# Kernel tuning notes

Hardware: AMD Instinct MI355X
Metric: run time of the kernel (lower is better)

The kernel has to match this reference:

```python
import jax, jax.numpy as jnp
import numpy as np

DIM = 256
WIN = 4
HEADS = 4
HEAD_DIM = DIM // HEADS
SCALE = HEAD_DIM ** (-0.5)


def setup_inputs() -> dict:
    key = jax.random.key(0)
    k1, k2, k3 = jax.random.split(key, 3)
    x = jax.random.normal(k1, (4, DIM, 32, 32, 32), dtype=jnp.float32)
    # xavier_uniform with gain=0.02 ~ small weights; scale approximated
    w_qkv = jax.random.normal(k2, (3 * DIM, DIM), dtype=jnp.float32) * 0.02
    w_proj = jax.random.normal(k3, (DIM, DIM), dtype=jnp.float32) * 0.02
    return {"x": x, "w_qkv": w_qkv, "w_proj": w_proj}


def reference(x, w_qkv, w_proj):
    B, C, D, H, W = x.shape
    N = D * H * W
    s = round(N ** (1.0 / 3.0))  # perfect cube asserted by original module
    w = WIN
    # (B,C,D,H,W) -> (B,N,C) -> (B,s,s,s,C)
    xt = x.reshape(B, C, N).transpose(0, 2, 1).reshape(B, s, s, s, C)
    pad = (w - s % w) % w
    if pad:
        xt = jnp.pad(xt, ((0, 0), (0, pad), (0, pad), (0, pad), (0, 0)))
    Sp = s + pad
    n = Sp // w  # windows per axis
    # torch unfold layout: (B, nD, nH, nW, C, w, w, w)
    xw = xt.reshape(B, n, w, n, w, n, w, C).transpose(0, 1, 3, 5, 7, 2, 4, 6)
    # faithful to torch .view(-1, w*w*w, C): row-major reinterpret of (C,w,w,w)
    xw = xw.reshape(-1, w * w * w, C)  # (nw, 64, C)
    nw, ntok = xw.shape[0], xw.shape[1]
    qkv = (xw @ w_qkv.T).reshape(nw, ntok, 3, HEADS, HEAD_DIM)
    q, k, v = qkv[:, :, 0], qkv[:, :, 1], qkv[:, :, 2]  # (nw, ntok, heads, hd)
    # faithful: NO head permute in original -> attention over the heads axis
    attn = jnp.einsum('wnhd,wngd->wnhg', q, k) * SCALE  # (nw, ntok, heads, heads)
    attn = jnp.clip(attn, -10.0, 10.0)
    attn = jax.nn.softmax(attn, axis=-1)
    out = jnp.einsum('wnhg,wngd->wnhd', attn, v)  # (nw, ntok, heads, hd)
    # faithful torch transpose(1,2).reshape(nw, ntok, dim)
    out = out.transpose(0, 2, 1, 3).reshape(nw, ntok, C)
    out = out @ w_proj.T
    out = out.reshape(B, n, n, n, w, w, w, C)
    out = out.transpose(0, 1, 4, 2, 5, 3, 6, 7).reshape(B, Sp, Sp, Sp, C)
    out = out[:, :s, :s, :s, :].transpose(0, 4, 1, 2, 3)  # (B,C,s,s,s)
    return out
```

## Files before the change

kernel.cpp:

```cpp
#include <hip/hip_runtime.h>

typedef _Float16 f16;
typedef f16 f16x2 __attribute__((ext_vector_type(2)));
typedef f16 f16x4 __attribute__((ext_vector_type(4)));
typedef f16 f16x8 __attribute__((ext_vector_type(8)));
typedef float f32x4 __attribute__((ext_vector_type(4)));

union v8split { f16x8 v8; f16x2 v2[4]; };

#define WQH_OFF 0
#define WPH_OFF (768 * 256 * 2)
#define XW_OFF  (WPH_OFF + 256 * 256 * 2)
#define O2_OFF  (XW_OFF + (size_t)2048 * 16384 * 2)
#define WS_NEED (O2_OFF + (size_t)2048 * 16384 * 2)

#define QKV_LDS_OFF 32768
#define SMEM_TOTAL 131072

__global__ __launch_bounds__(256) void cvt_weights_k(
    const float* __restrict__ wq, const float* __restrict__ wp,
    f16* __restrict__ wq_h, f16* __restrict__ wp_h) {
  int idx = blockIdx.x * 256 + threadIdx.x;
  if (idx < 768 * 256) wq_h[idx] = (f16)wq[idx];
  else wp_h[idx - 768 * 256] = (f16)wp[idx - 768 * 256];
}

__device__ __forceinline__ char* xwp(char* s, int row, int colbyte) {
  return s + row * 512 + (colbyte ^ (((row ^ (row >> 3)) & 7) << 4));
}
__device__ __forceinline__ char* qvp(char* s, int t, int fbyte) {
  return s + QKV_LDS_OFF + t * 1536 + (fbyte ^ ((t & 7) << 4));
}

__device__ __forceinline__ float qswapf(float v) {
  int x = __builtin_bit_cast(int, v);
  x = __builtin_amdgcn_update_dpp(0, x, 0xB1, 0xf, 0xf, true);
  return __builtin_bit_cast(float, x);
}

#if __has_builtin(__builtin_amdgcn_fdot2)
__device__ __forceinline__ float fdot2f(f16x2 a, f16x2 b, float c) {
  return __builtin_amdgcn_fdot2(a, b, c, false);
}
#else
__device__ __forceinline__ float fdot2f(f16x2 a, f16x2 b, float c) {
  return c + (float)a[0] * (float)b[0] + (float)a[1] * (float)b[1];
}
#endif

__global__ __launch_bounds__(256) void gather_k(const float* __restrict__ x,
                                                f16* __restrict__ xw_all) {
  const int g = blockIdx.x >> 4, cb = blockIdx.x & 15;
  const int b = g >> 6, iw = (g >> 3) & 7, jw = g & 7;
  const int tid = threadIdx.x;
  const int c = cb * 16 + (tid >> 4), a = (tid >> 2) & 3, bb = tid & 3;
  const float* src = x + (size_t)b * 8388608 + (size_t)c * 32768 +
                     (iw * 4 + a) * 1024 + (jw * 4 + bb) * 32;
  const int t = c >> 2;
  const int c2b = (c & 3) * 128 + a * 32 + bb * 8;
  const int byt = t * 512 + (c2b ^ (((t ^ (t >> 3)) & 7) << 4));
  char* wbase = (char*)(xw_all + (size_t)(g << 3) * 16384) + byt;
#pragma unroll
  for (int kw = 0; kw < 8; ++kw) {
    float4 v = *(const float4*)(src + kw * 4);
    f16x4 h;
    h[0] = (f16)v.x; h[1] = (f16)v.y; h[2] = (f16)v.z; h[3] = (f16)v.w;
    *(f16x4*)(wbase + kw * 32768) = h;
  }
}

__global__ __launch_bounds__(512) void win_attn_k(
    const f16* __restrict__ xw_all, const f16* __restrict__ wq_h,
    const f16* __restrict__ wp_h, f16* __restrict__ o2T) {
  extern __shared__ char smem[];
  const int wi = blockIdx.x;
  const int tid = threadIdx.x, wv = tid >> 6, lane = tid & 63;
  const int lcol = lane & 15, lq = lane >> 4;

  {
    const char* g = (const char*)(xw_all + (size_t)wi * 16384) + wv * 4096 + lane * 16;
#pragma unroll
    for (int i = 0; i < 4; ++i)
      __builtin_amdgcn_global_load_lds(
          (const __attribute__((address_space(1))) void*)(g + i * 1024),
          (__attribute__((address_space(3))) void*)(smem + wv * 4096 + i * 1024), 16, 0, 0);
  }
  __syncthreads();

#pragma unroll 1
  for (int half = 0; half < 2; ++half) {
    f32x4 acc[3][4] = {};
    const int fs = wv * 96 + half * 48;
#pragma unroll
    for (int kt = 0; kt < 8; ++kt) {
      f16x8 bf[4];
#pragma unroll
      for (int nt = 0; nt < 4; ++nt)
        bf[nt] = *(const f16x8*)xwp(smem, nt * 16 + lcol, kt * 64 + lq * 16);
#pragma unroll
      for (int ms = 0; ms < 3; ++ms) {
        f16x8 af = *(const f16x8*)(wq_h + (size_t)(fs + ms * 16 + lcol) * 256 + kt * 32 + lq * 8);
#pragma unroll
        for (int nt = 0; nt < 4; ++nt)
          acc[ms][nt] = __builtin_amdgcn_mfma_f32_16x16x32_f16(af, bf[nt], acc[ms][nt], 0, 0, 0);
      }
    }
#pragma unroll
    for (int ms = 0; ms < 3; ++ms)
#pragma unroll
      for (int nt = 0; nt < 4; ++nt) {
        f16x4 hv;
        hv[0] = (f16)acc[ms][nt][0]; hv[1] = (f16)acc[ms][nt][1];
        hv[2] = (f16)acc[ms][nt][2]; hv[3] = (f16)acc[ms][nt][3];
        *(f16x4*)qvp(smem, nt * 16 + lcol, (fs + ms * 16 + lq * 4) * 2) = hv;
      }
  }
  __syncthreads();

  {
    const int tt = lane >> 3, h = (lane >> 1) & 3, dh = lane & 1;
    const int t = wv * 8 + tt;
    const int db = dh * 64;

    f16x2 q2[16];
#pragma unroll
    for (int j = 0; j < 4; ++j) {
      v8split u;
      u.v8 = *(const f16x8*)qvp(smem, t, h * 128 + db + j * 16);
      q2[j * 4 + 0] = u.v2[0]; q2[j * 4 + 1] = u.v2[1];
      q2[j * 4 + 2] = u.v2[2]; q2[j * 4 + 3] = u.v2[3];
    }
    float s[4];
#pragma unroll
    for (int g = 0; g < 4; ++g) {
      float a = 0.f;
#pragma unroll
      for (int j = 0; j < 4; ++j) {
        v8split u;
        u.v8 = *(const f16x8*)qvp(smem, t, 512 + g * 128 + db + j * 16);
        a = fdot2f(q2[j * 4 + 0], u.v2[0], a);
        a = fdot2f(q2[j * 4 + 1], u.v2[1], a);
        a = fdot2f(q2[j * 4 + 2], u.v2[2], a);
        a = fdot2f(q2[j * 4 + 3], u.v2[3], a);
      }
      s[g] = a;
    }
#pragma unroll
    for (int g = 0; g < 4; ++g) s[g] += qswapf(s[g]);

    float mx = -1e30f;
#pragma unroll
    for (int g = 0; g < 4; ++g) {
      float v = fminf(fmaxf(s[g] * 0.125f, -10.f), 10.f);
      s[g] = v; mx = fmaxf(mx, v);
    }
    float sum = 0.f;
#pragma unroll
    for (int g = 0; g < 4; ++g) { s[g] = __expf(s[g] - mx); sum += s[g]; }
    float inv = 1.f / sum;
#pragma unroll
    for (int g = 0; g < 4; ++g) s[g] *= inv;

    float o[32] = {};
#pragma unroll
    for (int g = 0; g < 4; ++g) {
      float p = s[g];
#pragma unroll
      for (int j = 0; j < 4; ++j) {
        v8split u;
        u.v8 = *(const f16x8*)qvp(smem, t, 1024 + g * 128 + db + j * 16);
#pragma unroll
        for (int i = 0; i < 4; ++i) {
          o[j * 8 + 2 * i]     += p * (float)u.v2[i][0];
          o[j * 8 + 2 * i + 1] += p * (float)u.v2[i][1];
        }
      }
    }
    const int row = h * 16 + (t >> 2);
    const int cb0 = (t & 3) * 128 + db;
#pragma unroll
    for (int j = 0; j < 4; ++j) {
      f16x8 ov;
      ov[0] = (f16)o[j * 8 + 0]; ov[1] = (f16)o[j * 8 + 1];
      ov[2] = (f16)o[j * 8 + 2]; ov[3] = (f16)o[j * 8 + 3];
      ov[4] = (f16)o[j * 8 + 4]; ov[5] = (f16)o[j * 8 + 5];
      ov[6] = (f16)o[j * 8 + 6]; ov[7] = (f16)o[j * 8 + 7];
      *(f16x8*)xwp(smem, row, cb0 + j * 16) = ov;
    }
  }
  __syncthreads();

  {
    f32x4 acc2[4][2] = {};
#pragma unroll
    for (int kt = 0; kt < 8; ++kt) {
      f16x8 afr[4];
#pragma unroll
      for (int mt = 0; mt < 4; ++mt)
        afr[mt] = *(const f16x8*)xwp(smem, mt * 16 + lcol, kt * 64 + lq * 16);
#pragma unroll
      for (int nt = 0; nt < 2; ++nt) {
        f16x8 bfr = *(const f16x8*)(wp_h + (size_t)(wv * 32 + nt * 16 + lcol) * 256 + kt * 32 + lq * 8);
#pragma unroll
        for (int mt = 0; mt < 4; ++mt)
          acc2[mt][nt] = __builtin_amdgcn_mfma_f32_16x16x32_f16(afr[mt], bfr, acc2[mt][nt], 0, 0, 0);
      }
    }
    f16* ob = o2T + (size_t)wi * 16384;
#pragma unroll
    for (int mt = 0; mt < 4; ++mt)
#pragma unroll
      for (int nt = 0; nt < 2; ++nt) {
        int c3 = wv * 32 + nt * 16 + lcol;
        f16x4 hv;
        hv[0] = (f16)acc2[mt][nt][0]; hv[1] = (f16)acc2[mt][nt][1];
        hv[2] = (f16)acc2[mt][nt][2]; hv[3] = (f16)acc2[mt][nt][3];
        *(f16x4*)(ob + c3 * 64 + mt * 16 + lq * 4) = hv;
      }
  }
}

__global__ __launch_bounds__(256) void scatter_k(const f16* __restrict__ o2T,
                                                 float* __restrict__ out) {
  const int g = blockIdx.x >> 4, cb = blockIdx.x & 15;
  const int b = g >> 6, iw = (g >> 3) & 7, jw = g & 7;
  const int tid = threadIdx.x;
  const int c3 = cb * 16 + (tid >> 4), a = (tid >> 2) & 3, bb = tid & 3;
  const f16* rbase = o2T + (size_t)(g << 3) * 16384 + c3 * 64 + a * 16 + bb * 4;
  float* dst = out + (size_t)b * 8388608 + (size_t)c3 * 32768 +
               (iw * 4 + a) * 1024 + (jw * 4 + bb) * 32;
#pragma unroll
  for (int kw = 0; kw < 8; ++kw) {
    f16x4 h = *(const f16x4*)(rbase + kw * 16384);
    float4 v;
    v.x = (float)h[0]; v.y = (float)h[1]; v.z = (float)h[2]; v.w = (float)h[3];
    *(float4*)(dst + kw * 4) = v;
  }
}

#define FB_LDQ 68
#define FB_QKV_OFF 32768
#define FB_SPART_OFF (FB_QKV_OFF + 768 * FB_LDQ * 2)
#define FB_SMEM (FB_SPART_OFF + 32 * 64 * 4)

__device__ __forceinline__ char* fb_xwp(char* s, int row, int colbyte) {
  return s + row * 512 + (colbyte ^ ((row & 7) << 4));
}

__global__ __launch_bounds__(512) void fused_fb_k(
    const float* __restrict__ x, const f16* __restrict__ wq_h,
    const f16* __restrict__ wp_h, float* __restrict__ out) {
  extern __shared__ char smem[];
  f16* qkvT = (f16*)(smem + FB_QKV_OFF);
  float* spart = (float*)(smem + FB_SPART_OFF);
  const int tid = threadIdx.x;
  const int wi = blockIdx.x;
  const int kw = wi & 7, jw = (wi >> 3) & 7, iw = (wi >> 6) & 7, bw = wi >> 9;
  const float* xb = x + (size_t)bw * 8388608 + iw * 4096 + jw * 128 + kw * 4;
#pragma unroll
  for (int it = 0; it < 8; ++it) {
    int idx = it * 512 + tid;
    int c = idx >> 4, a = (idx >> 2) & 3, bb = idx & 3;
    float4 v = *(const float4*)(xb + (size_t)c * 32768 + a * 1024 + bb * 32);
    f16x4 h;
    h[0] = (f16)v.x; h[1] = (f16)v.y; h[2] = (f16)v.z; h[3] = (f16)v.w;
    *(f16x4*)fb_xwp(smem, c >> 2, (c & 3) * 128 + a * 32 + bb * 8) = h;
  }
  __syncthreads();
  const int wv = tid >> 6, lane = tid & 63;
  const int lcol = lane & 15, lq = lane >> 4;
  for (int nc = 0; nc < 2; ++nc) {
    const int ncb = wv * 96 + nc * 48;
    f32x4 acc[4][3] = {};
    for (int kt = 0; kt < 8; ++kt) {
      f16x8 afr[4];
#pragma unroll
      for (int mt = 0; mt < 4; ++mt)
        afr[mt] = *(const f16x8*)fb_xwp(smem, mt * 16 + lcol, kt * 64 + lq * 16);
#pragma unroll
      for (int nt = 0; nt < 3; ++nt) {
        f16x8 bfr = *(const f16x8*)(wq_h + (ncb + nt * 16 + lcol) * 256 + kt * 32 + lq * 8);
#pragma unroll
        for (int mt = 0; mt < 4; ++mt)
          acc[mt][nt] = __builtin_amdgcn_mfma_f32_16x16x32_f16(afr[mt], bfr, acc[mt][nt], 0, 0, 0);
      }
    }
#pragma unroll
    for (int mt = 0; mt < 4; ++mt)
#pragma unroll
      for (int nt = 0; nt < 3; ++nt) {
        f16x4 hv;
        hv[0] = (f16)acc[mt][nt][0]; hv[1] = (f16)acc[mt][nt][1];
        hv[2] = (f16)acc[mt][nt][2]; hv[3] = (f16)acc[mt][nt][3];
        *(f16x4*)(qkvT + (ncb + nt * 16 + lcol) * FB_LDQ + mt * 16 + lq * 4) = hv;
      }
  }
  __syncthreads();
  {
    const int h = wv & 3, dh = wv >> 2, t = lane;
    float qreg[32];
#pragma unroll
    for (int dd = 0; dd < 32; ++dd)
      qreg[dd] = (float)qkvT[(h * 64 + dh * 32 + dd) * FB_LDQ + t];
#pragma unroll
    for (int g = 0; g < 4; ++g) {
      float s = 0.f;
#pragma unroll
      for (int dd = 0; dd < 32; ++dd)
        s += qreg[dd] * (float)qkvT[(256 + g * 64 + dh * 32 + dd) * FB_LDQ + t];
      spart[((dh * 4 + h) * 4 + g) * 64 + t] = s;
    }
  }
  __syncthreads();
  {
    const int h = wv & 3, dh = wv >> 2, t = lane;
    float P[4];
    float mx = -1e30f;
#pragma unroll
    for (int g = 0; g < 4; ++g) {
      float s = spart[(h * 4 + g) * 64 + t] + spart[((4 + h) * 4 + g) * 64 + t];
      s *= 0.125f;
      s = fminf(fmaxf(s, -10.f), 10.f);
      P[g] = s;
      mx = fmaxf(mx, s);
    }
    float sum = 0.f;
#pragma unroll
    for (int g = 0; g < 4; ++g) { P[g] = __expf(P[g] - mx); sum += P[g]; }
    float inv = 1.f / sum;
#pragma unroll
    for (int g = 0; g < 4; ++g) P[g] *= inv;
    const int row = h * 16 + (t >> 2);
    const int cb0 = (t & 3) * 128 + dh * 64;
#pragma unroll
    for (int db = 0; db < 32; db += 8) {
      f16x8 hv;
#pragma unroll
      for (int u = 0; u < 8; ++u) {
        int d = dh * 32 + db + u;
        float o = 0.f;
#pragma unroll
        for (int g = 0; g < 4; ++g)
          o += P[g] * (float)qkvT[(512 + g * 64 + d) * FB_LDQ + t];
        hv[u] = (f16)o;
      }
      *(f16x8*)fb_xwp(smem, row, cb0 + db * 2) = hv;
    }
  }
  __syncthreads();
  {
    f32x4 acc[4][2] = {};
    for (int kt = 0; kt < 8; ++kt) {
      f16x8 afr[4];
#pragma unroll
      for (int mt = 0; mt < 4; ++mt)
        afr[mt] = *(const f16x8*)fb_xwp(smem, mt * 16 + lcol, kt * 64 + lq * 16);
#pragma unroll
      for (int nt = 0; nt < 2; ++nt) {
        f16x8 bfr = *(const f16x8*)(wp_h + (wv * 32 + nt * 16 + lcol) * 256 + kt * 32 + lq * 8);
#pragma unroll
        for (int mt = 0; mt < 4; ++mt)
          acc[mt][nt] = __builtin_amdgcn_mfma_f32_16x16x32_f16(afr[mt], bfr, acc[mt][nt], 0, 0, 0);
      }
    }
    float* ob = out + (size_t)bw * 8388608 + iw * 4096 + jw * 128 + kw * 4;
#pragma unroll
    for (int mt = 0; mt < 4; ++mt) {
#pragma unroll
      for (int nt = 0; nt < 2; ++nt) {
        int c3 = wv * 32 + nt * 16 + lcol;
        float4 v;
        v.x = acc[mt][nt][0]; v.y = acc[mt][nt][1];
        v.z = acc[mt][nt][2]; v.w = acc[mt][nt][3];
        *(float4*)(ob + (size_t)c3 * 32768 + mt * 1024 + lq * 32) = v;
      }
    }
  }
}

extern "C" void kernel_launch(void* const* d_in, const int* in_sizes, int n_in,
                              void* d_out, int out_size, void* d_ws, size_t ws_size,
                              hipStream_t stream) {
  const float* x = (const float*)d_in[0];
  const float* wq = (const float*)d_in[1];
  const float* wp = (const float*)d_in[2];
  float* out = (float*)d_out;
  char* ws = (char*)d_ws;
  f16* wq_h = (f16*)(ws + WQH_OFF);
  f16* wp_h = (f16*)(ws + WPH_OFF);

  cvt_weights_k<<<1024, 256, 0, stream>>>(wq, wp, wq_h, wp_h);

  if (ws_size >= WS_NEED) {
    f16* xw_all = (f16*)(ws + XW_OFF);
    f16* o2T = (f16*)(ws + O2_OFF);
    (void)hipFuncSetAttribute((const void*)win_attn_k,
                              hipFuncAttributeMaxDynamicSharedMemorySize, SMEM_TOTAL);
    gather_k<<<4096, 256, 0, stream>>>(x, xw_all);
    win_attn_k<<<2048, 512, SMEM_TOTAL, stream>>>(xw_all, wq_h, wp_h, o2T);
    scatter_k<<<4096, 256, 0, stream>>>(o2T, out);
  } else {
    (void)hipFuncSetAttribute((const void*)fused_fb_k,
                              hipFuncAttributeMaxDynamicSharedMemorySize, FB_SMEM);
    fused_fb_k<<<2048, 512, FB_SMEM, stream>>>(x, wq_h, wp_h, out);
  }
}
```

Before: 268.6 us.

## Split each attention window across two blocks with half-size LDS

Each window's 64 tokens are split between two workgroups of 32 tokens each. The grid doubles to 4096 blocks and LDS per block halves to 64 KB, which should allow more resident blocks per CU and better latency hiding. The gather layout, the QKV/attention lane mapping (now four lanes per head with a two-step DPP reduction) and the output indexing are all reworked to match. The cost is that both blocks of a window reload the same weight tiles, doubling weight traffic from L2, and each block issues fewer MFMAs per weight fragment it loads.

```diff
diff --git a/kernel.cpp b/kernel.cpp
--- a/kernel.cpp
+++ b/kernel.cpp
@@ -14,8 +14,8 @@
 #define O2_OFF  (XW_OFF + (size_t)2048 * 16384 * 2)
 #define WS_NEED (O2_OFF + (size_t)2048 * 16384 * 2)
 
-#define QKV_LDS_OFF 32768
-#define SMEM_TOTAL 131072
+#define QKV_LDS_OFF 16384
+#define SMEM_TOTAL 65536
 
 __global__ __launch_bounds__(256) void cvt_weights_k(
     const float* __restrict__ wq, const float* __restrict__ wp,
@@ -32,9 +32,14 @@
   return s + QKV_LDS_OFF + t * 1536 + (fbyte ^ ((t & 7) << 4));
 }
 
-__device__ __forceinline__ float qswapf(float v) {
+__device__ __forceinline__ float qswap1f(float v) {
   int x = __builtin_bit_cast(int, v);
   x = __builtin_amdgcn_update_dpp(0, x, 0xB1, 0xf, 0xf, true);
+  return __builtin_bit_cast(float, x);
+}
+__device__ __forceinline__ float qswap2f(float v) {
+  int x = __builtin_bit_cast(int, v);
+  x = __builtin_amdgcn_update_dpp(0, x, 0x4E, 0xf, 0xf, true);
   return __builtin_bit_cast(float, x);
 }
 
@@ -56,16 +61,16 @@
   const int c = cb * 16 + (tid >> 4), a = (tid >> 2) & 3, bb = tid & 3;
   const float* src = x + (size_t)b * 8388608 + (size_t)c * 32768 +
                      (iw * 4 + a) * 1024 + (jw * 4 + bb) * 32;
-  const int t = c >> 2;
+  const int t = c >> 2, hb = t >> 5, tl = t & 31;
   const int c2b = (c & 3) * 128 + a * 32 + bb * 8;
-  const int byt = t * 512 + (c2b ^ (((t ^ (t >> 3)) & 7) << 4));
-  char* wbase = (char*)(xw_all + (size_t)(g << 3) * 16384) + byt;
+  const int byt = tl * 512 + (c2b ^ (((tl ^ (tl >> 3)) & 7) << 4));
+  char* wbase = (char*)(xw_all + (size_t)(g * 16 + hb) * 8192) + byt;
 #pragma unroll
   for (int kw = 0; kw < 8; ++kw) {
     float4 v = *(const float4*)(src + kw * 4);
     f16x4 h;
     h[0] = (f16)v.x; h[1] = (f16)v.y; h[2] = (f16)v.z; h[3] = (f16)v.w;
-    *(f16x4*)(wbase + kw * 32768) = h;
+    *(f16x4*)(wbase + (size_t)kw * 32768) = h;
   }
 }
 
@@ -73,42 +78,44 @@
     const f16* __restrict__ xw_all, const f16* __restrict__ wq_h,
     const f16* __restrict__ wp_h, f16* __restrict__ o2T) {
   extern __shared__ char smem[];
-  const int wi = blockIdx.x;
+  const int hw = blockIdx.x;
+  const int wi = hw >> 1, hb = hw & 1;
   const int tid = threadIdx.x, wv = tid >> 6, lane = tid & 63;
   const int lcol = lane & 15, lq = lane >> 4;
 
   {
-    const char* g = (const char*)(xw_all + (size_t)wi * 16384) + wv * 4096 + lane * 16;
-#pragma unroll
-    for (int i = 0; i < 4; ++i)
+    const char* g = (const char*)(xw_all + (size_t)hw * 8192) + tid * 16;
+#pragma unroll
+    for (int i = 0; i < 2; ++i)
       __builtin_amdgcn_global_load_lds(
-          (const __attribute__((address_space(1))) void*)(g + i * 1024),
-          (__attribute__((address_space(3))) void*)(smem + wv * 4096 + i * 1024), 16, 0, 0);
+          (const __attribute__((address_space(1))) void*)(g + i * 8192),
+          (__attribute__((address_space(3))) void*)(smem + tid * 16 + i * 8192),
+          16, 0, 0);
   }
   __syncthreads();
 
 #pragma unroll 1
   for (int half = 0; half < 2; ++half) {
-    f32x4 acc[3][4] = {};
+    f32x4 acc[3][2] = {};
     const int fs = wv * 96 + half * 48;
 #pragma unroll
     for (int kt = 0; kt < 8; ++kt) {
-      f16x8 bf[4];
-#pragma unroll
-      for (int nt = 0; nt < 4; ++nt)
+      f16x8 bf[2];
+#pragma unroll
+      for (int nt = 0; nt < 2; ++nt)
         bf[nt] = *(const f16x8*)xwp(smem, nt * 16 + lcol, kt * 64 + lq * 16);
 #pragma unroll
       for (int ms = 0; ms < 3; ++ms) {
         f16x8 af = *(const f16x8*)(wq_h + (size_t)(fs + ms * 16 + lcol) * 256 + kt * 32 + lq * 8);
 #pragma unroll
-        for (int nt = 0; nt < 4; ++nt)
+        for (int nt = 0; nt < 2; ++nt)
           acc[ms][nt] = __builtin_amdgcn_mfma_f32_16x16x32_f16(af, bf[nt], acc[ms][nt], 0, 0, 0);
       }
     }
 #pragma unroll
     for (int ms = 0; ms < 3; ++ms)
 #pragma unroll
-      for (int nt = 0; nt < 4; ++nt) {
+      for (int nt = 0; nt < 2; ++nt) {
         f16x4 hv;
         hv[0] = (f16)acc[ms][nt][0]; hv[1] = (f16)acc[ms][nt][1];
         hv[2] = (f16)acc[ms][nt][2]; hv[3] = (f16)acc[ms][nt][3];
@@ -118,15 +125,15 @@
   __syncthreads();
 
   {
-    const int tt = lane >> 3, h = (lane >> 1) & 3, dh = lane & 1;
-    const int t = wv * 8 + tt;
-    const int db = dh * 64;
-
-    f16x2 q2[16];
-#pragma unroll
-    for (int j = 0; j < 4; ++j) {
+    const int tt = lane >> 4, h = (lane >> 2) & 3, dq = lane & 3;
+    const int tl = wv * 4 + tt;
+    const int db = dq * 32;
+
+    f16x2 q2[8];
+#pragma unroll
+    for (int j = 0; j < 2; ++j) {
       v8split u;
-      u.v8 = *(const f16x8*)qvp(smem, t, h * 128 + db + j * 16);
+      u.v8 = *(const f16x8*)qvp(smem, tl, h * 128 + db + j * 16);
       q2[j * 4 + 0] = u.v2[0]; q2[j * 4 + 1] = u.v2[1];
       q2[j * 4 + 2] = u.v2[2]; q2[j * 4 + 3] = u.v2[3];
     }
@@ -135,9 +142,9 @@
     for (int g = 0; g < 4; ++g) {
       float a = 0.f;
 #pragma unroll
-      for (int j = 0; j < 4; ++j) {
+      for (int j = 0; j < 2; ++j) {
         v8split u;
-        u.v8 = *(const f16x8*)qvp(smem, t, 512 + g * 128 + db + j * 16);
+        u.v8 = *(const f16x8*)qvp(smem, tl, 512 + g * 128 + db + j * 16);
         a = fdot2f(q2[j * 4 + 0], u.v2[0], a);
         a = fdot2f(q2[j * 4 + 1], u.v2[1], a);
         a = fdot2f(q2[j * 4 + 2], u.v2[2], a);
@@ -146,7 +153,10 @@
       s[g] = a;
     }
 #pragma unroll
-    for (int g = 0; g < 4; ++g) s[g] += qswapf(s[g]);
+    for (int g = 0; g < 4; ++g) {
+      s[g] += qswap1f(s[g]);
+      s[g] += qswap2f(s[g]);
+    }
 
     float mx = -1e30f;
 #pragma unroll
@@ -161,14 +171,14 @@
 #pragma unroll
     for (int g = 0; g < 4; ++g) s[g] *= inv;
 
-    float o[32] = {};
+    float o[16] = {};
 #pragma unroll
     for (int g = 0; g < 4; ++g) {
       float p = s[g];
 #pragma unroll
-      for (int j = 0; j < 4; ++j) {
+      for (int j = 0; j < 2; ++j) {
         v8split u;
-        u.v8 = *(const f16x8*)qvp(smem, t, 1024 + g * 128 + db + j * 16);
+        u.v8 = *(const f16x8*)qvp(smem, tl, 1024 + g * 128 + db + j * 16);
 #pragma unroll
         for (int i = 0; i < 4; ++i) {
           o[j * 8 + 2 * i]     += p * (float)u.v2[i][0];
@@ -176,10 +186,10 @@
         }
       }
     }
-    const int row = h * 16 + (t >> 2);
-    const int cb0 = (t & 3) * 128 + db;
-#pragma unroll
-    for (int j = 0; j < 4; ++j) {
+    const int row = h * 8 + (tl >> 2);
+    const int cb0 = (tl & 3) * 128 + db;
+#pragma unroll
+    for (int j = 0; j < 2; ++j) {
       f16x8 ov;
       ov[0] = (f16)o[j * 8 + 0]; ov[1] = (f16)o[j * 8 + 1];
       ov[2] = (f16)o[j * 8 + 2]; ov[3] = (f16)o[j * 8 + 3];
@@ -191,31 +201,33 @@
   __syncthreads();
 
   {
-    f32x4 acc2[4][2] = {};
+    f32x4 acc2[2][2] = {};
 #pragma unroll
     for (int kt = 0; kt < 8; ++kt) {
-      f16x8 afr[4];
-#pragma unroll
-      for (int mt = 0; mt < 4; ++mt)
+      f16x8 afr[2];
+#pragma unroll
+      for (int mt = 0; mt < 2; ++mt)
         afr[mt] = *(const f16x8*)xwp(smem, mt * 16 + lcol, kt * 64 + lq * 16);
 #pragma unroll
       for (int nt = 0; nt < 2; ++nt) {
         f16x8 bfr = *(const f16x8*)(wp_h + (size_t)(wv * 32 + nt * 16 + lcol) * 256 + kt * 32 + lq * 8);
 #pragma unroll
-        for (int mt = 0; mt < 4; ++mt)
+        for (int mt = 0; mt < 2; ++mt)
           acc2[mt][nt] = __builtin_amdgcn_mfma_f32_16x16x32_f16(afr[mt], bfr, acc2[mt][nt], 0, 0, 0);
       }
     }
     f16* ob = o2T + (size_t)wi * 16384;
-#pragma unroll
-    for (int mt = 0; mt < 4; ++mt)
+    const int t2b = hb * 8 + ((lq & 1) * 4);
+#pragma unroll
+    for (int mt = 0; mt < 2; ++mt)
 #pragma unroll
       for (int nt = 0; nt < 2; ++nt) {
         int c3 = wv * 32 + nt * 16 + lcol;
+        int t2 = (mt * 2 + (lq >> 1)) * 16 + t2b;
         f16x4 hv;
         hv[0] = (f16)acc2[mt][nt][0]; hv[1] = (f16)acc2[mt][nt][1];
         hv[2] = (f16)acc2[mt][nt][2]; hv[3] = (f16)acc2[mt][nt][3];
-        *(f16x4*)(ob + c3 * 64 + mt * 16 + lq * 4) = hv;
+        *(f16x4*)(ob + c3 * 64 + t2) = hv;
       }
   }
 }
@@ -397,7 +409,7 @@
     (void)hipFuncSetAttribute((const void*)win_attn_k,
                               hipFuncAttributeMaxDynamicSharedMemorySize, SMEM_TOTAL);
     gather_k<<<4096, 256, 0, stream>>>(x, xw_all);
-    win_attn_k<<<2048, 512, SMEM_TOTAL, stream>>>(xw_all, wq_h, wp_h, o2T);
+    win_attn_k<<<4096, 512, SMEM_TOTAL, stream>>>(xw_all, wq_h, wp_h, o2T);
     scatter_k<<<4096, 256, 0, stream>>>(o2T, out);
   } else {
     (void)hipFuncSetAttribute((const void*)fused_fb_k,
```

New measurement: 383.0 us. +42.6%, slower.

## Double win_attn_k block size to 1024 threads, splitting work across 16 waves

Applied to the files above, without the earlier changes.

Launches the window-attention kernel with 1024 threads (16 waves) per window instead of 512. The QKV GEMM drops the two-pass half loop so each wave computes 48 features once. The attention stage splits each head across four lanes with a two-step DPP reduction, and the projection GEMM gives each wave 16 output channels. The goal is more parallelism and latency hiding per window, since LDS use (128KB) limits residency to one block per CU. The cost is more waves contending for LDS and more redundant shared-memory reads of the projection A fragments.

```diff
diff --git a/kernel.cpp b/kernel.cpp
--- a/kernel.cpp
+++ b/kernel.cpp
@@ -32,9 +32,14 @@
   return s + QKV_LDS_OFF + t * 1536 + (fbyte ^ ((t & 7) << 4));
 }
 
-__device__ __forceinline__ float qswapf(float v) {
+__device__ __forceinline__ float qswap1f(float v) {
   int x = __builtin_bit_cast(int, v);
   x = __builtin_amdgcn_update_dpp(0, x, 0xB1, 0xf, 0xf, true);
+  return __builtin_bit_cast(float, x);
+}
+__device__ __forceinline__ float qswap2f(float v) {
+  int x = __builtin_bit_cast(int, v);
+  x = __builtin_amdgcn_update_dpp(0, x, 0x4E, 0xf, 0xf, true);
   return __builtin_bit_cast(float, x);
 }
 
@@ -69,7 +74,7 @@
   }
 }
 
-__global__ __launch_bounds__(512) void win_attn_k(
+__global__ __launch_bounds__(1024) void win_attn_k(
     const f16* __restrict__ xw_all, const f16* __restrict__ wq_h,
     const f16* __restrict__ wp_h, f16* __restrict__ o2T) {
   extern __shared__ char smem[];
@@ -78,19 +83,19 @@
   const int lcol = lane & 15, lq = lane >> 4;
 
   {
-    const char* g = (const char*)(xw_all + (size_t)wi * 16384) + wv * 4096 + lane * 16;
-#pragma unroll
-    for (int i = 0; i < 4; ++i)
-      __builtin_amdgcn_global_load_lds(
-          (const __attribute__((address_space(1))) void*)(g + i * 1024),
-          (__attribute__((address_space(3))) void*)(smem + wv * 4096 + i * 1024), 16, 0, 0);
-  }
-  __syncthreads();
-
-#pragma unroll 1
-  for (int half = 0; half < 2; ++half) {
+    const char* g = (const char*)(xw_all + (size_t)wi * 16384) + tid * 16;
+    __builtin_amdgcn_global_load_lds(
+        (const __attribute__((address_space(1))) void*)(g),
+        (__attribute__((address_space(3))) void*)(smem + tid * 16), 16, 0, 0);
+    __builtin_amdgcn_global_load_lds(
+        (const __attribute__((address_space(1))) void*)(g + 16384),
+        (__attribute__((address_space(3))) void*)(smem + tid * 16 + 16384), 16, 0, 0);
+  }
+  __syncthreads();
+
+  {
     f32x4 acc[3][4] = {};
-    const int fs = wv * 96 + half * 48;
+    const int fs = wv * 48;
 #pragma unroll
     for (int kt = 0; kt < 8; ++kt) {
       f16x8 bf[4];
@@ -118,13 +123,13 @@
   __syncthreads();
 
   {
-    const int tt = lane >> 3, h = (lane >> 1) & 3, dh = lane & 1;
-    const int t = wv * 8 + tt;
-    const int db = dh * 64;
-
-    f16x2 q2[16];
-#pragma unroll
-    for (int j = 0; j < 4; ++j) {
+    const int tt = lane >> 4, h = (lane >> 2) & 3, dq = lane & 3;
+    const int t = wv * 4 + tt;
+    const int db = dq * 32;
+
+    f16x2 q2[8];
+#pragma unroll
+    for (int j = 0; j < 2; ++j) {
       v8split u;
       u.v8 = *(const f16x8*)qvp(smem, t, h * 128 + db + j * 16);
       q2[j * 4 + 0] = u.v2[0]; q2[j * 4 + 1] = u.v2[1];
@@ -135,7 +140,7 @@
     for (int g = 0; g < 4; ++g) {
       float a = 0.f;
 #pragma unroll
-      for (int j = 0; j < 4; ++j) {
+      for (int j = 0; j < 2; ++j) {
         v8split u;
         u.v8 = *(const f16x8*)qvp(smem, t, 512 + g * 128 + db + j * 16);
         a = fdot2f(q2[j * 4 + 0], u.v2[0], a);
@@ -146,7 +151,10 @@
       s[g] = a;
     }
 #pragma unroll
-    for (int g = 0; g < 4; ++g) s[g] += qswapf(s[g]);
+    for (int g = 0; g < 4; ++g) {
+      s[g] += qswap1f(s[g]);
+      s[g] += qswap2f(s[g]);
+    }
 
     float mx = -1e30f;
 #pragma unroll
@@ -161,12 +169,12 @@
 #pragma unroll
     for (int g = 0; g < 4; ++g) s[g] *= inv;
 
-    float o[32] = {};
+    float o[16] = {};
 #pragma unroll
     for (int g = 0; g < 4; ++g) {
       float p = s[g];
 #pragma unroll
-      for (int j = 0; j < 4; ++j) {
+      for (int j = 0; j < 2; ++j) {
         v8split u;
         u.v8 = *(const f16x8*)qvp(smem, t, 1024 + g * 128 + db + j * 16);
 #pragma unroll
@@ -179,7 +187,7 @@
     const int row = h * 16 + (t >> 2);
     const int cb0 = (t & 3) * 128 + db;
 #pragma unroll
-    for (int j = 0; j < 4; ++j) {
+    for (int j = 0; j < 2; ++j) {
       f16x8 ov;
       ov[0] = (f16)o[j * 8 + 0]; ov[1] = (f16)o[j * 8 + 1];
       ov[2] = (f16)o[j * 8 + 2]; ov[3] = (f16)o[j * 8 + 3];
@@ -191,32 +199,26 @@
   __syncthreads();
 
   {
-    f32x4 acc2[4][2] = {};
+    f32x4 acc2[4] = {};
+    const int c3 = wv * 16 + lcol;
+    const f16* bp = wp_h + (size_t)c3 * 256;
 #pragma unroll
     for (int kt = 0; kt < 8; ++kt) {
-      f16x8 afr[4];
-#pragma unroll
-      for (int mt = 0; mt < 4; ++mt)
-        afr[mt] = *(const f16x8*)xwp(smem, mt * 16 + lcol, kt * 64 + lq * 16);
-#pragma unroll
-      for (int nt = 0; nt < 2; ++nt) {
-        f16x8 bfr = *(const f16x8*)(wp_h + (size_t)(wv * 32 + nt * 16 + lcol) * 256 + kt * 32 + lq * 8);
-#pragma unroll
-        for (int mt = 0; mt < 4; ++mt)
-          acc2[mt][nt] = __builtin_amdgcn_mfma_f32_16x16x32_f16(afr[mt], bfr, acc2[mt][nt], 0, 0, 0);
+      f16x8 bfr = *(const f16x8*)(bp + kt * 32 + lq * 8);
+#pragma unroll
+      for (int mt = 0; mt < 4; ++mt) {
+        f16x8 afr = *(const f16x8*)xwp(smem, mt * 16 + lcol, kt * 64 + lq * 16);
+        acc2[mt] = __builtin_amdgcn_mfma_f32_16x16x32_f16(afr, bfr, acc2[mt], 0, 0, 0);
       }
     }
     f16* ob = o2T + (size_t)wi * 16384;
 #pragma unroll
-    for (int mt = 0; mt < 4; ++mt)
-#pragma unroll
-      for (int nt = 0; nt < 2; ++nt) {
-        int c3 = wv * 32 + nt * 16 + lcol;
-        f16x4 hv;
-        hv[0] = (f16)acc2[mt][nt][0]; hv[1] = (f16)acc2[mt][nt][1];
-        hv[2] = (f16)acc2[mt][nt][2]; hv[3] = (f16)acc2[mt][nt][3];
-        *(f16x4*)(ob + c3 * 64 + mt * 16 + lq * 4) = hv;
-      }
+    for (int mt = 0; mt < 4; ++mt) {
+      f16x4 hv;
+      hv[0] = (f16)acc2[mt][0]; hv[1] = (f16)acc2[mt][1];
+      hv[2] = (f16)acc2[mt][2]; hv[3] = (f16)acc2[mt][3];
+      *(f16x4*)(ob + c3 * 64 + mt * 16 + lq * 4) = hv;
+    }
   }
 }
 
@@ -397,7 +399,7 @@
     (void)hipFuncSetAttribute((const void*)win_attn_k,
                               hipFuncAttributeMaxDynamicSharedMemorySize, SMEM_TOTAL);
     gather_k<<<4096, 256, 0, stream>>>(x, xw_all);
-    win_attn_k<<<2048, 512, SMEM_TOTAL, stream>>>(xw_all, wq_h, wp_h, o2T);
+    win_attn_k<<<2048, 1024, SMEM_TOTAL, stream>>>(xw_all, wq_h, wp_h, o2T);
     scatter_k<<<4096, 256, 0, stream>>>(o2T, out);
   } else {
     (void)hipFuncSetAttribute((const void*)fused_fb_k,
```

Result: no change. 270.6 us (+0.7%).
